# Performance work log

Measured on AMD Instinct MI355X. Metric: run time of the kernel, lower is better.

Reference implementation:

```python
import jax, jax.numpy as jnp
import numpy as np

N_QUBITS = 7
N_LAYERS = 2
DIM = 2 ** N_QUBITS  # 128
NORM_FACTOR = 1.0


def _cnot_gather_idx(n):
    # CNOT chain (0,1),(1,2),...,(n-2,n-1) plus wraparound (n-1,0).
    # new_state[x] = old_state[idx[x]]; apply gates in reverse to arange.
    gates = [(i, i + 1) for i in range(n - 1)] + [(n - 1, 0)]
    idx = np.arange(2 ** n)
    for c, t in reversed(gates):
        cbit = 1 << (n - 1 - c)  # pennylane wire 0 = most significant bit
        tbit = 1 << (n - 1 - t)
        idx = np.where((idx & cbit) > 0, idx ^ tbit, idx)
    return jnp.asarray(idx)

CNOT_IDX = _cnot_gather_idx(N_QUBITS)


def silu(x):
    return x * jax.nn.sigmoid(x)


def cayley(A_real, A_imag):
    # Hermitianize then Cayley transform -> unitary, per layer. [L,D,D]
    A = A_real.astype(jnp.complex64) + 1j * A_imag.astype(jnp.complex64)
    A = A + jnp.conj(jnp.swapaxes(A, -1, -2))
    I = jnp.eye(DIM, dtype=A.dtype)
    return jnp.matmul(A - 1j * I, jnp.linalg.inv(A + 1j * I))


def _single_qubit_gate(theta_x, theta_y):
    # combined G = RY(theta_y) @ RX(theta_x) applied to every qubit
    cx, sx = jnp.cos(theta_x / 2), jnp.sin(theta_x / 2)
    cy, sy = jnp.cos(theta_y / 2), jnp.sin(theta_y / 2)
    RX = jnp.stack([jnp.stack([cx + 0j, -1j * sx]), jnp.stack([-1j * sx, cx + 0j])])
    RY = jnp.stack([jnp.stack([cy + 0j, -sy + 0j]), jnp.stack([sy + 0j, cy + 0j])])
    return RY @ RX


def quantum_evolve(psi, coeffs, q_mats):
    # psi: [N, DIM] complex64 normalized state vectors
    N = psi.shape[0]
    for j in range(N_LAYERS):
        psi = psi @ q_mats[j].T  # QubitUnitary: new = U @ old
        G = _single_qubit_gate(coeffs[j, 0], coeffs[j, 1])
        psi = psi.reshape((N,) + (2,) * N_QUBITS)
        for ax in range(1, N_QUBITS + 1):
            psi = jnp.moveaxis(jnp.tensordot(G, psi, axes=((1,), (ax,))), 0, ax)
        psi = psi.reshape(N, DIM)
        psi = psi[:, CNOT_IDX]  # CNOT chain is a fixed basis permutation
    return psi


def setup_inputs() -> dict:
    key = jax.random.key(0)
    ks = jax.random.split(key, 16)
    N, E = 50000, 800000
    in_nf, hid, out_nf = 128, 128, 128
    h = jax.random.normal(ks[0], (N, in_nf), dtype=jnp.float32)
    edge_index = jax.random.randint(ks[1], (2, E), 0, N)
    s = 0.05
    W_e1 = jax.random.normal(ks[2], (2 * in_nf, hid), dtype=jnp.float32) * s
    b_e1 = jnp.zeros((hid,), dtype=jnp.float32)
    W_e2 = jax.random.normal(ks[3], (hid, hid), dtype=jnp.float32) * s
    b_e2 = jnp.zeros((hid,), dtype=jnp.float32)
    W_enc = jax.random.normal(ks[4], (hid + in_nf, DIM), dtype=jnp.float32) * s
    b_enc = jnp.zeros((DIM,), dtype=jnp.float32)
    coeffs = jax.random.normal(ks[5], (N_LAYERS, 2), dtype=jnp.float32) * 0.1
    A_real = jax.random.normal(ks[6], (N_LAYERS, DIM, DIM), dtype=jnp.float32) * 0.01
    A_imag = jax.random.normal(ks[7], (N_LAYERS, DIM, DIM), dtype=jnp.float32) * 0.01
    W_dec = jax.random.normal(ks[8], (DIM, out_nf), dtype=jnp.float32) * s
    b_dec = jnp.zeros((out_nf,), dtype=jnp.float32)
    return {"h": h, "edge_index": edge_index, "W_e1": W_e1, "b_e1": b_e1,
            "W_e2": W_e2, "b_e2": b_e2, "W_enc": W_enc, "b_enc": b_enc,
            "coeffs": coeffs, "A_real": A_real, "A_imag": A_imag,
            "W_dec": W_dec, "b_dec": b_dec}


def reference(h, edge_index, W_e1, b_e1, W_e2, b_e2, W_enc, b_enc,
              coeffs, A_real, A_imag, W_dec, b_dec):
    row, col = edge_index[0], edge_index[1]
    # edge model: mij = MLP([h_src, h_tgt])
    e = jnp.concatenate([h[row], h[col]], axis=1)  # [E, 2*in_nf]
    e = silu(e @ W_e1 + b_e1)
    edge_feat = silu(e @ W_e2 + b_e2)  # [E, hid]
    # node model: scatter-sum aggregation over destination `row`
    agg = jax.ops.segment_sum(edge_feat, row, num_segments=h.shape[0]) / NORM_FACTOR
    q_input = jnp.concatenate([h, agg], axis=1) @ W_enc + b_enc  # [N, DIM]
    norm = jnp.sqrt(jnp.sum(q_input ** 2, axis=1, keepdims=True) + 1e-12)
    psi = (q_input / norm).astype(jnp.complex64)
    q_mats = cayley(A_real, A_imag)  # [L, DIM, DIM] unitary
    psi = quantum_evolve(psi, coeffs, q_mats)
    out = h + (jnp.real(psi) @ W_dec + b_dec)
    return out, edge_feat
```

## Files before the change

kernel.cpp:

```cpp
#include <hip/hip_runtime.h>
#include <math.h>

#define N_NODES 50000
#define N_EDGES 800000

typedef __attribute__((ext_vector_type(8))) short bf16x8;
typedef __attribute__((ext_vector_type(4))) short bf16x4;
typedef __attribute__((ext_vector_type(2))) short shortx2;
typedef __attribute__((ext_vector_type(4))) float f32x4;

__device__ __forceinline__ float silu_f(float x) {
    float d = 1.0f + __expf(-x);
    return x * __builtin_amdgcn_rcpf(d);
}

__device__ __forceinline__ unsigned short f2bf(float x) {
    union { float f; unsigned u; } v; v.f = x;
    unsigned r = v.u + 0x7FFFu + ((v.u >> 16) & 1u);
    return (unsigned short)(r >> 16);
}

__device__ __forceinline__ void atomic_pk_add_bf16(short* addr, shortx2 v) {
    typedef shortx2 __attribute__((address_space(1)))* gp1;
    __builtin_amdgcn_global_atomic_fadd_v2bf16((gp1)(unsigned long long)addr, v);
}

__global__ __launch_bounds__(256) void prep_kernel(const float* __restrict__ h,
                                                   short* __restrict__ hbf,
                                                   const int* __restrict__ ei,
                                                   int* __restrict__ cnt,
                                                   const float* __restrict__ A_real,
                                                   const float* __restrict__ A_imag,
                                                   float* __restrict__ H,
                                                   float* __restrict__ X) {
    const int bid = blockIdx.x;
    const int t = threadIdx.x;
    if (bid < 3125) {
        int i = bid * 256 + t;
        const float4* h4 = (const float4*)h;
        float4 v0 = h4[i * 2], v1 = h4[i * 2 + 1];
        bf16x8 b;
        b[0] = (short)f2bf(v0.x); b[1] = (short)f2bf(v0.y);
        b[2] = (short)f2bf(v0.z); b[3] = (short)f2bf(v0.w);
        b[4] = (short)f2bf(v1.x); b[5] = (short)f2bf(v1.y);
        b[6] = (short)f2bf(v1.z); b[7] = (short)f2bf(v1.w);
        ((bf16x8*)hbf)[i] = b;
        atomicAdd(&cnt[ei[i]], 1);
    } else {
        int p = bid - 3125;
        int L = p >> 2, q4 = p & 3;
        const float* ar = A_real + L * 16384;
        const float* ai = A_imag + L * 16384;
        float* hre = H + L * 32768;
        float* him = hre + 16384;
        float* xre = X + L * 32768;
        float* xim = xre + 16384;
        for (int m = 0; m < 16; ++m) {
            int idx = q4 * 4096 + t + 256 * m;
            int i = idx >> 7, j = idx & 127;
            float hr = ar[idx] + ar[j * 128 + i];
            float hi = ai[idx] - ai[j * 128 + i];
            hre[idx] = hr;
            him[idx] = hi;
            xre[idx] = hr;
            xim[idx] = hi - (i == j ? 1.0f : 0.0f);
        }
    }
}

__device__ __forceinline__ void ns_t_body(int blk, int t,
                                          const float* __restrict__ H,
                                          const float* __restrict__ X,
                                          float* __restrict__ T) {
    const int L = blk >> 4;
    const int i = (blk & 15) * 8 + (t >> 7);
    const int j = t & 127;
    const float* hre = H + L * 32768;
    const float* him = hre + 16384;
    const float* xre = X + L * 32768;
    const float* xim = xre + 16384;
    float accr = 0.f, acci = 0.f;
    #pragma unroll 4
    for (int k = 0; k < 128; ++k) {
        float hr = hre[i * 128 + k], hi = him[i * 128 + k];
        float xr = xre[k * 128 + j], xi = xim[k * 128 + j];
        accr += hr * xr - hi * xi;
        acci += hr * xi + hi * xr;
    }
    T[L * 32768 + i * 128 + j]          = accr - xim[i * 128 + j];
    T[L * 32768 + 16384 + i * 128 + j]  = acci + xre[i * 128 + j];
}

__device__ __forceinline__ void ns_x_body(int blk, int t,
                                          const float* __restrict__ X,
                                          const float* __restrict__ T,
                                          float* __restrict__ Xout) {
    const int L = blk >> 4;
    const int i = (blk & 15) * 8 + (t >> 7);
    const int j = t & 127;
    const float* xre = X + L * 32768;
    const float* xim = xre + 16384;
    const float* tre = T + L * 32768;
    const float* tim = tre + 16384;
    float accr = 0.f, acci = 0.f;
    #pragma unroll 4
    for (int k = 0; k < 128; ++k) {
        float xr = xre[i * 128 + k], xi = xim[i * 128 + k];
        float tr = tre[k * 128 + j], ti = tim[k * 128 + j];
        accr += xr * tr - xi * ti;
        acci += xr * ti + xi * tr;
    }
    Xout[L * 32768 + i * 128 + j]          = 2.0f * xre[i * 128 + j] - accr;
    Xout[L * 32768 + 16384 + i * 128 + j]  = 2.0f * xim[i * 128 + j] - acci;
}

__global__ __launch_bounds__(1024) void nst_scan_kernel(const float* __restrict__ H,
                                                        const float* __restrict__ X,
                                                        float* __restrict__ T,
                                                        const int* __restrict__ cnt,
                                                        int* __restrict__ cursor) {
    const int bid = blockIdx.x;
    const int t = threadIdx.x;
    if (bid < 32) { ns_t_body(bid, t, H, X, T); return; }
    __shared__ int sA[1024];
    __shared__ int sB[1024];
    const int CH = 49;
    int s = 0;
    #pragma unroll 4
    for (int i = 0; i < CH; ++i) {
        int idx = t * CH + i;
        if (idx < N_NODES) s += cnt[idx];
    }
    sA[t] = s;
    __syncthreads();
    int* src = sA;
    int* dst = sB;
    for (int off = 1; off < 1024; off <<= 1) {
        int v = src[t];
        if (t >= off) v += src[t - off];
        dst[t] = v;
        __syncthreads();
        int* tmp = src; src = dst; dst = tmp;
    }
    int run = (t == 0) ? 0 : src[t - 1];
    for (int i = 0; i < CH; ++i) {
        int idx = t * CH + i;
        if (idx < N_NODES) {
            cursor[idx] = run;
            run += cnt[idx];
        }
    }
}

__global__ __launch_bounds__(1024) void fill_nsx_kernel(const int* __restrict__ ei,
                                                        int* __restrict__ cursor,
                                                        int* __restrict__ elist,
                                                        const float* __restrict__ X,
                                                        const float* __restrict__ T,
                                                        float* __restrict__ Xout) {
    const int bid = blockIdx.x;
    const int t = threadIdx.x;
    if (bid < 782) {
        int e = bid * 1024 + t;
        if (e < N_EDGES) {
            int slot = atomicAdd(&cursor[ei[e]], 1);
            elist[slot] = e;
        }
        return;
    }
    ns_x_body(bid - 782, t, X, T, Xout);
}

__global__ __launch_bounds__(1024) void ns_t_kernel(const float* __restrict__ H,
                                                    const float* __restrict__ X,
                                                    float* __restrict__ T) {
    ns_t_body(blockIdx.x, threadIdx.x, H, X, T);
}

__global__ __launch_bounds__(1024) void ns_x_kernel(const float* __restrict__ X,
                                                    const float* __restrict__ T,
                                                    float* __restrict__ Xout) {
    ns_x_body(blockIdx.x, threadIdx.x, X, T, Xout);
}

__global__ __launch_bounds__(1024) void gateperm_kernel(const float* __restrict__ X,
                                                        const float* __restrict__ coeffs,
                                                        float* __restrict__ Y) {
    __shared__ float Mre[128 * 129];
    __shared__ float Mim[128 * 129];
    const int L = blockIdx.x;
    const int t = threadIdx.x;
    const float* xre = X + L * 32768;
    const float* xim = xre + 16384;

    for (int q = 0; q < 16; ++q) {
        int idx = t + 1024 * q;
        int i = idx >> 7, j = idx & 127;
        Mre[i * 129 + j] = (i == j ? 1.0f : 0.0f) + 2.0f * xim[idx];
        Mim[i * 129 + j] = -2.0f * xre[idx];
    }
    __syncthreads();

    const float tx = coeffs[2 * L + 0] * 0.5f;
    const float ty = coeffs[2 * L + 1] * 0.5f;
    const float cx = cosf(tx), sx = sinf(tx), cy = cosf(ty), sy = sinf(ty);
    const float G00r = cx * cy, G00i = sx * sy;
    const float G01r = -cx * sy, G01i = -sx * cy;
    const float G10r = cx * sy, G10i = -sx * cy;
    const float G11r = cx * cy, G11i = -sx * sy;

    for (int st = 0; st < 7; ++st) {
        int b = 1 << st;
        #pragma unroll
        for (int p = 0; p < 8; ++p) {
            int pid = t + 1024 * p;
            int col = pid & 127, ph = pid >> 7;
            int i0 = ((ph >> st) << (st + 1)) | (ph & (b - 1));
            int i1 = i0 | b;
            float v0r = Mre[i0 * 129 + col], v0i = Mim[i0 * 129 + col];
            float v1r = Mre[i1 * 129 + col], v1i = Mim[i1 * 129 + col];
            Mre[i0 * 129 + col] = G00r * v0r - G00i * v0i + G01r * v1r - G01i * v1i;
            Mim[i0 * 129 + col] = G00r * v0i + G00i * v0r + G01r * v1i + G01i * v1r;
            Mre[i1 * 129 + col] = G10r * v0r - G10i * v0i + G11r * v1r - G11i * v1i;
            Mim[i1 * 129 + col] = G10r * v0i + G10i * v0r + G11r * v1i + G11i * v1r;
        }
        __syncthreads();
    }

    const int cs[7] = {6, 5, 4, 3, 2, 1, 0};
    const int ts[7] = {0, 6, 5, 4, 3, 2, 1};
    float* yre = Y + L * 32768;
    float* yim = yre + 16384;
    for (int q = 0; q < 16; ++q) {
        int idx = t + 1024 * q;
        int ii_ = idx >> 7, col = idx & 127;
        int s = ii_;
        #pragma unroll
        for (int m = 0; m < 7; ++m) {
            int cbit = 1 << (6 - cs[m]);
            int tbit = 1 << (6 - ts[m]);
            if (s & cbit) s ^= tbit;
        }
        yre[idx] = Mre[s * 129 + col];
        yim[idx] = Mim[s * 129 + col];
    }
}

__global__ __launch_bounds__(512) void combine1_kernel(const float* __restrict__ Y,
                                                       float* __restrict__ ReM) {
    __shared__ float q1r[16384];
    __shared__ float q1i[16384];
    const int t = threadIdx.x;
    const float* q1re = Y;
    const float* q1im = Y + 16384;
    const float* q2re = Y + 32768;
    const float* q2im = Y + 49152;
    for (int q = 0; q < 32; ++q) {
        q1r[t + 512 * q] = q1re[t + 512 * q];
        q1i[t + 512 * q] = q1im[t + 512 * q];
    }
    __syncthreads();
    int i = blockIdx.x * 4 + (t >> 7);
    int j = t & 127;
    float acc = 0.f;
    for (int k = 0; k < 128; ++k) {
        acc += q2re[i * 128 + k] * q1r[k * 128 + j] - q2im[i * 128 + k] * q1i[k * 128 + j];
    }
    ReM[i * 128 + j] = acc;
}

__global__ __launch_bounds__(512) void combine2_kernel(const float* __restrict__ ReM,
                                                       const float* __restrict__ W_dec,
                                                       short* __restrict__ Dt) {
    __shared__ float ml[16384];
    __shared__ float wl[16384];
    const int t = threadIdx.x;
    for (int q = 0; q < 32; ++q) {
        ml[t + 512 * q] = ReM[t + 512 * q];
        wl[t + 512 * q] = W_dec[t + 512 * q];
    }
    __syncthreads();
    int k = blockIdx.x * 4 + (t >> 7);
    int j = t & 127;
    float acc = 0.f;
    for (int i = 0; i < 128; ++i) {
        acc += ml[i * 128 + k] * wl[i * 128 + j];
    }
    Dt[j * 128 + k] = (short)f2bf(acc);
}

__global__ __launch_bounds__(768)
__attribute__((amdgpu_waves_per_eu(3, 3)))
void edge_kernel(const short* __restrict__ hbf,
                 const int* __restrict__ ei,
                 const int* __restrict__ elist,
                 const float* __restrict__ W_e1,
                 const float* __restrict__ b_e1,
                 const float* __restrict__ W_e2,
                 const float* __restrict__ b_e2,
                 float* __restrict__ ef_out,
                 short* __restrict__ agg_bf) {
    __shared__ short w1f[64 * 64 * 8];
    __shared__ short w2f[32 * 64 * 8];
    __shared__ short c1s[12][16 * 68];

    const int t = threadIdx.x;
    const int lane = t & 63;
    const int w = t >> 6;
    const int l15 = lane & 15;
    const int kg = lane >> 4;

    {
        const float4* w1_4 = (const float4*)W_e1;
        for (int idx4 = t; idx4 < 8192; idx4 += 768) {
            int k = idx4 >> 5, j4 = idx4 & 31;
            float4 v = w1_4[idx4];
            int s = k >> 5, kgs = (k >> 3) & 3, e = k & 7;
            int fb = s * 8;
            float vz[4] = {v.x, v.y, v.z, v.w};
            #pragma unroll
            for (int z = 0; z < 4; ++z) {
                int j = j4 * 4 + z;
                int nf = j >> 4, jl = j & 15;
                w1f[((fb + nf) * 64 + kgs * 16 + jl) * 8 + e] = (short)f2bf(vz[z]);
            }
        }
        const float4* w2_4 = (const float4*)W_e2;
        for (int idx4 = t; idx4 < 4096; idx4 += 768) {
            int k = idx4 >> 5, j4 = idx4 & 31;
            float4 v = w2_4[idx4];
            int s2 = k >> 5, kgs = (k >> 3) & 3, e = k & 7;
            int fb = s2 * 8;
            float vz[4] = {v.x, v.y, v.z, v.w};
            #pragma unroll
            for (int z = 0; z < 4; ++z) {
                int j = j4 * 4 + z;
                int nf = j >> 4, jl = j & 15;
                w2f[((fb + nf) * 64 + kgs * 16 + jl) * 8 + e] = (short)f2bf(vz[z]);
            }
        }
    }
    float b1v[8], b2v[8];
    #pragma unroll
    for (int nf = 0; nf < 8; ++nf) {
        b1v[nf] = b_e1[nf * 16 + l15];
        b2v[nf] = b_e2[nf * 16 + l15];
    }
    __syncthreads();

    const bf16x8* hb8 = (const bf16x8*)hbf;
    const bf16x8* w1v = (const bf16x8*)w1f;
    const bf16x8* w2v = (const bf16x8*)w2f;
    short* myc1 = &c1s[w][0];
    const int nt = N_EDGES / 16;
    const int TW = gridDim.x * 12;
    const int wvid = blockIdx.x * 12 + w;
    int tile = (int)(((long long)nt * wvid) / TW);
    const int tend = (int)(((long long)nt * (wvid + 1)) / TW);
    if (tile >= tend) return;

    int el = elist[tile * 16 + l15];
    int ri = ei[el];
    int ci = ei[N_EDGES + el];
    bf16x8 a1[8];
    #pragma unroll
    for (int s = 0; s < 4; ++s) a1[s] = hb8[(size_t)ri * 16 + s * 4 + kg];
    #pragma unroll
    for (int s = 0; s < 4; ++s) a1[4 + s] = hb8[(size_t)ci * 16 + s * 4 + kg];

    bool hn = (tile + 1 < tend);
    int eln = 0, rin = 0, cin = 0;
    if (hn) {
        eln = elist[(tile + 1) * 16 + l15];
        rin = ei[eln];
        cin = ei[N_EDGES + eln];
    }

    float runsum[8];
    #pragma unroll
    for (int nf = 0; nf < 8; ++nf) runsum[nf] = 0.f;

    for (;;) {
        bool hn2 = (tile + 2 < tend);
        int eln2 = 0, rin2 = 0, cin2 = 0;
        if (hn2) {
            eln2 = elist[(tile + 2) * 16 + l15];
            rin2 = ei[eln2];
            cin2 = ei[N_EDGES + eln2];
        }

        f32x4 acc[8];
        #pragma unroll
        for (int nf = 0; nf < 8; ++nf) acc[nf] = (f32x4){0.f, 0.f, 0.f, 0.f};
        #pragma unroll
        for (int s = 0; s < 8; ++s) {
            #pragma unroll
            for (int nf = 0; nf < 8; ++nf) {
                bf16x8 b = w1v[(s * 8 + nf) * 64 + lane];
                acc[nf] = __builtin_amdgcn_mfma_f32_16x16x32_bf16(a1[s], b, acc[nf], 0, 0, 0);
            }
        }

        bf16x8 a1n[8];
        if (hn) {
            #pragma unroll
            for (int s = 0; s < 4; ++s) a1n[s] = hb8[(size_t)rin * 16 + s * 4 + kg];
            #pragma unroll
            for (int s = 0; s < 4; ++s) a1n[4 + s] = hb8[(size_t)cin * 16 + s * 4 + kg];
        }

        f32x4 acc2[8];
        #pragma unroll
        for (int nf = 0; nf < 8; ++nf) acc2[nf] = (f32x4){0.f, 0.f, 0.f, 0.f};
        #pragma unroll
        for (int half = 0; half < 2; ++half) {
            #pragma unroll
            for (int nfh = 0; nfh < 4; ++nfh) {
                int nf = half * 4 + nfh;
                #pragma unroll
                for (int r = 0; r < 4; ++r) {
                    int row = kg * 4 + r;
                    int c = nfh * 16 + l15;
                    myc1[row * 68 + c] = (short)f2bf(silu_f(acc[nf][r] + b1v[nf]));
                }
            }
            #pragma unroll
            for (int s2l = 0; s2l < 2; ++s2l) {
                int k0h = s2l * 32 + kg * 8;
                int base = l15 * 68 + k0h;
                bf16x4 lo = *(const bf16x4*)&myc1[base];
                bf16x4 hi = *(const bf16x4*)&myc1[base + 4];
                bf16x8 a2;
                #pragma unroll
                for (int z = 0; z < 4; ++z) { a2[z] = lo[z]; a2[4 + z] = hi[z]; }
                int s2 = half * 2 + s2l;
                #pragma unroll
                for (int nf = 0; nf < 8; ++nf) {
                    bf16x8 b = w2v[(s2 * 8 + nf) * 64 + lane];
                    acc2[nf] = __builtin_amdgcn_mfma_f32_16x16x32_bf16(a2, b, acc2[nf], 0, 0, 0);
                }
            }
        }

        int rw[4], ew[4];
        #pragma unroll
        for (int r = 0; r < 4; ++r) {
            rw[r] = __shfl(ri, kg * 4 + r);
            ew[r] = __shfl(el, kg * 4 + r);
        }
        int rwn0 = hn ? __shfl(rin, kg * 4) : -1;
        #pragma unroll
        for (int r = 0; r < 4; ++r) {
            float* efp = ef_out + (size_t)ew[r] * 128;
            #pragma unroll
            for (int nf = 0; nf < 8; ++nf) {
                int col = nf * 16 + l15;
                float v = silu_f(acc2[nf][r] + b2v[nf]);
                __builtin_nontemporal_store(v, efp + col);
                runsum[nf] += v;
            }
            bool end = (r < 3) ? (rw[r + 1] != rw[r]) : (rw[3] != rwn0);
            if (end) {
                short* agp = agg_bf + (size_t)rw[r] * 128;
                #pragma unroll
                for (int nf = 0; nf < 8; ++nf) {
                    float vn = __shfl_xor(runsum[nf], 1);
                    if ((l15 & 1) == 0) {
                        shortx2 pk;
                        pk.x = (short)f2bf(runsum[nf]);
                        pk.y = (short)f2bf(vn);
                        atomic_pk_add_bf16(agp + nf * 16 + l15, pk);
                    }
                    runsum[nf] = 0.f;
                }
            }
        }

        if (!hn) break;
        tile += 1;
        el = eln; ri = rin; ci = cin;
        #pragma unroll
        for (int s = 0; s < 8; ++s) a1[s] = a1n[s];
        hn = hn2; eln = eln2; rin = rin2; cin = cin2;
    }
}

__global__ __launch_bounds__(1024)
__attribute__((amdgpu_waves_per_eu(4, 4)))
void node_kernel(const short* __restrict__ hbf,
                 const short* __restrict__ agg_bf,
                 const float* __restrict__ W_enc,
                 const float* __restrict__ b_enc,
                 const short* __restrict__ Dt_bf,
                 const float* __restrict__ b_dec,
                 const float* __restrict__ h,
                 float* __restrict__ out) {
    __shared__ short wef[64 * 64 * 8];
    __shared__ short dtf[32 * 64 * 8];
    __shared__ short c1s[16][16 * 68];

    const int t = threadIdx.x;
    const int lane = t & 63;
    const int w = t >> 6;
    const int l15 = lane & 15;
    const int kg = lane >> 4;

    {
        const float4* we4 = (const float4*)W_enc;
        for (int idx4 = t; idx4 < 8192; idx4 += 1024) {
            int k = idx4 >> 5, j4 = idx4 & 31;
            float4 v = we4[idx4];
            int s = k >> 5, kgs = (k >> 3) & 3, e = k & 7;
            int fb = s * 8;
            float vz[4] = {v.x, v.y, v.z, v.w};
            #pragma unroll
            for (int z = 0; z < 4; ++z) {
                int j = j4 * 4 + z;
                int nf = j >> 4, jl = j & 15;
                wef[((fb + nf) * 64 + kgs * 16 + jl) * 8 + e] = (short)f2bf(vz[z]);
            }
        }
        const bf16x8* dt8 = (const bf16x8*)Dt_bf;
        bf16x8* dtv = (bf16x8*)dtf;
        for (int idx8 = t; idx8 < 2048; idx8 += 1024) {
            int brow = idx8 >> 4, kslot = idx8 & 15;
            int s2 = kslot >> 2, kgs = kslot & 3;
            int nf = brow >> 4, jl = brow & 15;
            dtv[(s2 * 8 + nf) * 64 + kgs * 16 + jl] = dt8[idx8];
        }
    }
    float bj1[8], bj2[8];
    #pragma unroll
    for (int nf = 0; nf < 8; ++nf) {
        bj1[nf] = b_enc[nf * 16 + l15];
        bj2[nf] = b_dec[nf * 16 + l15];
    }
    __syncthreads();

    const bf16x8* hb8 = (const bf16x8*)hbf;
    const bf16x8* ab8 = (const bf16x8*)agg_bf;
    const bf16x8* wev = (const bf16x8*)wef;
    const bf16x8* dtv = (const bf16x8*)dtf;
    short* myc1 = &c1s[w][0];
    const int nt = N_NODES / 16;
    const int tile = blockIdx.x * 16 + w;
    if (tile >= nt) return;

    const int node = tile * 16 + l15;
    bf16x8 a[8];
    #pragma unroll
    for (int s = 0; s < 4; ++s) a[s] = hb8[(size_t)node * 16 + s * 4 + kg];
    #pragma unroll
    for (int s = 0; s < 4; ++s) a[4 + s] = ab8[(size_t)node * 16 + s * 4 + kg];

    f32x4 acc[8];
    #pragma unroll
    for (int nf = 0; nf < 8; ++nf) acc[nf] = (f32x4){0.f, 0.f, 0.f, 0.f};
    #pragma unroll
    for (int s = 0; s < 8; ++s) {
        #pragma unroll
        for (int nf = 0; nf < 8; ++nf) {
            bf16x8 b = wev[(s * 8 + nf) * 64 + lane];
            acc[nf] = __builtin_amdgcn_mfma_f32_16x16x32_bf16(a[s], b, acc[nf], 0, 0, 0);
        }
    }

    float nr[4] = {0.f, 0.f, 0.f, 0.f};
    #pragma unroll
    for (int nf = 0; nf < 8; ++nf) {
        #pragma unroll
        for (int r = 0; r < 4; ++r) {
            acc[nf][r] += bj1[nf];
            nr[r] += acc[nf][r] * acc[nf][r];
        }
    }
    #pragma unroll
    for (int r = 0; r < 4; ++r) {
        nr[r] += __shfl_xor(nr[r], 1);
        nr[r] += __shfl_xor(nr[r], 2);
        nr[r] += __shfl_xor(nr[r], 4);
        nr[r] += __shfl_xor(nr[r], 8);
        nr[r] = 1.0f / sqrtf(nr[r] + 1e-12f);
    }

    f32x4 acc2[8];
    #pragma unroll
    for (int nf = 0; nf < 8; ++nf) acc2[nf] = (f32x4){0.f, 0.f, 0.f, 0.f};
    #pragma unroll
    for (int half = 0; half < 2; ++half) {
        #pragma unroll
        for (int nfh = 0; nfh < 4; ++nfh) {
            int nf = half * 4 + nfh;
            #pragma unroll
            for (int r = 0; r < 4; ++r) {
                int row = kg * 4 + r;
                int c = nfh * 16 + l15;
                myc1[row * 68 + c] = (short)f2bf(acc[nf][r] * nr[r]);
            }
        }
        #pragma unroll
        for (int s2l = 0; s2l < 2; ++s2l) {
            int k0h = s2l * 32 + kg * 8;
            int base = l15 * 68 + k0h;
            bf16x4 lo = *(const bf16x4*)&myc1[base];
            bf16x4 hi = *(const bf16x4*)&myc1[base + 4];
            bf16x8 a2;
            #pragma unroll
            for (int z = 0; z < 4; ++z) { a2[z] = lo[z]; a2[4 + z] = hi[z]; }
            int s2 = half * 2 + s2l;
            #pragma unroll
            for (int nf = 0; nf < 8; ++nf) {
                bf16x8 b = dtv[(s2 * 8 + nf) * 64 + lane];
                acc2[nf] = __builtin_amdgcn_mfma_f32_16x16x32_bf16(a2, b, acc2[nf], 0, 0, 0);
            }
        }
    }

    #pragma unroll
    for (int r = 0; r < 4; ++r) {
        size_t rowb = (size_t)(tile * 16 + kg * 4 + r) * 128;
        #pragma unroll
        for (int nf = 0; nf < 8; ++nf) {
            int col = nf * 16 + l15;
            out[rowb + col] = h[rowb + col] + acc2[nf][r] + bj2[nf];
        }
    }
}

extern "C" void kernel_launch(void* const* d_in, const int* in_sizes, int n_in,
                              void* d_out, int out_size, void* d_ws, size_t ws_size,
                              hipStream_t stream) {
    const float* h      = (const float*)d_in[0];
    const int*   ei     = (const int*)d_in[1];
    const float* W_e1   = (const float*)d_in[2];
    const float* b_e1   = (const float*)d_in[3];
    const float* W_e2   = (const float*)d_in[4];
    const float* b_e2   = (const float*)d_in[5];
    const float* W_enc  = (const float*)d_in[6];
    const float* b_enc  = (const float*)d_in[7];
    const float* coeffs = (const float*)d_in[8];
    const float* A_real = (const float*)d_in[9];
    const float* A_imag = (const float*)d_in[10];
    const float* W_dec  = (const float*)d_in[11];
    const float* b_dec  = (const float*)d_in[12];

    float* out    = (float*)d_out;
    float* ef_out = out + (size_t)N_NODES * 128;

    short* agg_bf = (short*)d_ws;
    int*   cnt    = (int*)(agg_bf + (size_t)N_NODES * 128);
    short* h_bf   = (short*)(cnt + 50176);
    int*   cursor = (int*)(h_bf + (size_t)N_NODES * 128);
    int*   elist  = cursor + 50176;
    float* small  = (float*)(elist + N_EDGES);
    float* Ybuf   = small;
    float* ReM    = Ybuf + 65536;
    float* Hbuf   = ReM + 16384;
    float* Xa     = Hbuf + 65536;
    float* Xb     = Xa + 65536;
    float* Tbuf   = Xb + 65536;
    short* Dt_bf  = (short*)(Tbuf + 65536);

    hipMemsetAsync(agg_bf, 0, (size_t)N_NODES * 128 * sizeof(short) + 50176 * sizeof(int),
                   stream);

    prep_kernel<<<3133, 256, 0, stream>>>(h, h_bf, ei, cnt, A_real, A_imag, Hbuf, Xa);
    nst_scan_kernel<<<33, 1024, 0, stream>>>(Hbuf, Xa, Tbuf, cnt, cursor);
    fill_nsx_kernel<<<814, 1024, 0, stream>>>(ei, cursor, elist, Xa, Tbuf, Xb);
    ns_t_kernel<<<32, 1024, 0, stream>>>(Hbuf, Xb, Tbuf);
    ns_x_kernel<<<32, 1024, 0, stream>>>(Xb, Tbuf, Xa);

    gateperm_kernel<<<2, 1024, 0, stream>>>(Xa, coeffs, Ybuf);
    combine1_kernel<<<32, 512, 0, stream>>>(Ybuf, ReM);
    combine2_kernel<<<32, 512, 0, stream>>>(ReM, W_dec, Dt_bf);

    edge_kernel<<<256, 768, 0, stream>>>(h_bf, ei, elist, W_e1, b_e1, W_e2, b_e2,
                                         ef_out, agg_bf);

    node_kernel<<<196, 1024, 0, stream>>>(h_bf, agg_bf, W_enc, b_enc, Dt_bf, b_dec, h, out);
}
```

Baseline: 593.6 us.

## Process two 16-edge tiles per wave in edge kernel to reuse weight fragments

Each wave now handles 32 edges per iteration as two interleaved 16-row MFMA tiles, so every LDS weight fragment load feeds two MFMAs instead of one. The block shrinks from 12 to 8 waves with waves_per_eu lowered to 2, giving more registers per wave. The previous one-tile-ahead prefetch of node feature rows is dropped: gathers now load at the top of each iteration, and only the next tile's edge indices are prefetched. This exposes more gather latency and lowers occupancy in exchange for halving LDS weight traffic per edge.

```diff
diff --git a/kernel.cpp b/kernel.cpp
--- a/kernel.cpp
+++ b/kernel.cpp
@@ -289,8 +289,8 @@
     Dt[j * 128 + k] = (short)f2bf(acc);
 }
 
-__global__ __launch_bounds__(768)
-__attribute__((amdgpu_waves_per_eu(3, 3)))
+__global__ __launch_bounds__(512)
+__attribute__((amdgpu_waves_per_eu(2, 2)))
 void edge_kernel(const short* __restrict__ hbf,
                  const int* __restrict__ ei,
                  const int* __restrict__ elist,
@@ -302,7 +302,7 @@
                  short* __restrict__ agg_bf) {
     __shared__ short w1f[64 * 64 * 8];
     __shared__ short w2f[32 * 64 * 8];
-    __shared__ short c1s[12][16 * 68];
+    __shared__ short c1s[8][32 * 68];
 
     const int t = threadIdx.x;
     const int lane = t & 63;
@@ -312,7 +312,7 @@
 
     {
         const float4* w1_4 = (const float4*)W_e1;
-        for (int idx4 = t; idx4 < 8192; idx4 += 768) {
+        for (int idx4 = t; idx4 < 8192; idx4 += 512) {
             int k = idx4 >> 5, j4 = idx4 & 31;
             float4 v = w1_4[idx4];
             int s = k >> 5, kgs = (k >> 3) & 3, e = k & 7;
@@ -326,7 +326,7 @@
             }
         }
         const float4* w2_4 = (const float4*)W_e2;
-        for (int idx4 = t; idx4 < 4096; idx4 += 768) {
+        for (int idx4 = t; idx4 < 4096; idx4 += 512) {
             int k = idx4 >> 5, j4 = idx4 & 31;
             float4 v = w2_4[idx4];
             int s2 = k >> 5, kgs = (k >> 3) & 3, e = k & 7;
@@ -352,66 +352,63 @@
     const bf16x8* w1v = (const bf16x8*)w1f;
     const bf16x8* w2v = (const bf16x8*)w2f;
     short* myc1 = &c1s[w][0];
-    const int nt = N_EDGES / 16;
-    const int TW = gridDim.x * 12;
-    const int wvid = blockIdx.x * 12 + w;
+    const int nt = N_EDGES / 32;
+    const int TW = gridDim.x * 8;
+    const int wvid = blockIdx.x * 8 + w;
     int tile = (int)(((long long)nt * wvid) / TW);
     const int tend = (int)(((long long)nt * (wvid + 1)) / TW);
     if (tile >= tend) return;
 
-    int el = elist[tile * 16 + l15];
-    int ri = ei[el];
-    int ci = ei[N_EDGES + el];
-    bf16x8 a1[8];
-    #pragma unroll
-    for (int s = 0; s < 4; ++s) a1[s] = hb8[(size_t)ri * 16 + s * 4 + kg];
-    #pragma unroll
-    for (int s = 0; s < 4; ++s) a1[4 + s] = hb8[(size_t)ci * 16 + s * 4 + kg];
-
-    bool hn = (tile + 1 < tend);
-    int eln = 0, rin = 0, cin = 0;
-    if (hn) {
-        eln = elist[(tile + 1) * 16 + l15];
-        rin = ei[eln];
-        cin = ei[N_EDGES + eln];
-    }
-
-    float runsum[8];
-    #pragma unroll
-    for (int nf = 0; nf < 8; ++nf) runsum[nf] = 0.f;
+    int el0 = elist[tile * 32 + l15];
+    int el1 = elist[tile * 32 + 16 + l15];
+    int ri0 = ei[el0], ci0 = ei[N_EDGES + el0];
+    int ri1 = ei[el1], ci1 = ei[N_EDGES + el1];
+
+    float rs0[8], rs1[8];
+    #pragma unroll
+    for (int nf = 0; nf < 8; ++nf) { rs0[nf] = 0.f; rs1[nf] = 0.f; }
 
     for (;;) {
-        bool hn2 = (tile + 2 < tend);
-        int eln2 = 0, rin2 = 0, cin2 = 0;
-        if (hn2) {
-            eln2 = elist[(tile + 2) * 16 + l15];
-            rin2 = ei[eln2];
-            cin2 = ei[N_EDGES + eln2];
-        }
-
-        f32x4 acc[8];
-        #pragma unroll
-        for (int nf = 0; nf < 8; ++nf) acc[nf] = (f32x4){0.f, 0.f, 0.f, 0.f};
+        bf16x8 aA[8], aB[8];
+        #pragma unroll
+        for (int s = 0; s < 4; ++s) {
+            aA[s]     = hb8[(size_t)ri0 * 16 + s * 4 + kg];
+            aA[4 + s] = hb8[(size_t)ci0 * 16 + s * 4 + kg];
+            aB[s]     = hb8[(size_t)ri1 * 16 + s * 4 + kg];
+            aB[4 + s] = hb8[(size_t)ci1 * 16 + s * 4 + kg];
+        }
+
+        const bool hn = (tile + 1 < tend);
+        int el0n = 0, el1n = 0, ri0n = 0, ci0n = 0, ri1n = 0, ci1n = 0;
+        if (hn) {
+            el0n = elist[(tile + 1) * 32 + l15];
+            el1n = elist[(tile + 1) * 32 + 16 + l15];
+            ri0n = ei[el0n]; ci0n = ei[N_EDGES + el0n];
+            ri1n = ei[el1n]; ci1n = ei[N_EDGES + el1n];
+        }
+
+        f32x4 acc0[8], acc1[8];
+        #pragma unroll
+        for (int nf = 0; nf < 8; ++nf) {
+            acc0[nf] = (f32x4){0.f, 0.f, 0.f, 0.f};
+            acc1[nf] = (f32x4){0.f, 0.f, 0.f, 0.f};
+        }
         #pragma unroll
         for (int s = 0; s < 8; ++s) {
             #pragma unroll
             for (int nf = 0; nf < 8; ++nf) {
                 bf16x8 b = w1v[(s * 8 + nf) * 64 + lane];
-                acc[nf] = __builtin_amdgcn_mfma_f32_16x16x32_bf16(a1[s], b, acc[nf], 0, 0, 0);
-            }
-        }
-
-        bf16x8 a1n[8];
-        if (hn) {
-            #pragma unroll
-            for (int s = 0; s < 4; ++s) a1n[s] = hb8[(size_t)rin * 16 + s * 4 + kg];
-            #pragma unroll
-            for (int s = 0; s < 4; ++s) a1n[4 + s] = hb8[(size_t)cin * 16 + s * 4 + kg];
-        }
-
-        f32x4 acc2[8];
-        #pragma unroll
-        for (int nf = 0; nf < 8; ++nf) acc2[nf] = (f32x4){0.f, 0.f, 0.f, 0.f};
+                acc0[nf] = __builtin_amdgcn_mfma_f32_16x16x32_bf16(aA[s], b, acc0[nf], 0, 0, 0);
+                acc1[nf] = __builtin_amdgcn_mfma_f32_16x16x32_bf16(aB[s], b, acc1[nf], 0, 0, 0);
+            }
+        }
+
+        f32x4 acc20[8], acc21[8];
+        #pragma unroll
+        for (int nf = 0; nf < 8; ++nf) {
+            acc20[nf] = (f32x4){0.f, 0.f, 0.f, 0.f};
+            acc21[nf] = (f32x4){0.f, 0.f, 0.f, 0.f};
+        }
         #pragma unroll
         for (int half = 0; half < 2; ++half) {
             #pragma unroll
@@ -421,67 +418,111 @@
                 for (int r = 0; r < 4; ++r) {
                     int row = kg * 4 + r;
                     int c = nfh * 16 + l15;
-                    myc1[row * 68 + c] = (short)f2bf(silu_f(acc[nf][r] + b1v[nf]));
+                    myc1[row * 68 + c] = (short)f2bf(silu_f(acc0[nf][r] + b1v[nf]));
+                    myc1[(16 + row) * 68 + c] = (short)f2bf(silu_f(acc1[nf][r] + b1v[nf]));
                 }
             }
             #pragma unroll
             for (int s2l = 0; s2l < 2; ++s2l) {
                 int k0h = s2l * 32 + kg * 8;
-                int base = l15 * 68 + k0h;
-                bf16x4 lo = *(const bf16x4*)&myc1[base];
-                bf16x4 hi = *(const bf16x4*)&myc1[base + 4];
-                bf16x8 a2;
+                int base0 = l15 * 68 + k0h;
+                int base1 = (16 + l15) * 68 + k0h;
+                bf16x4 lo0 = *(const bf16x4*)&myc1[base0];
+                bf16x4 hi0 = *(const bf16x4*)&myc1[base0 + 4];
+                bf16x4 lo1 = *(const bf16x4*)&myc1[base1];
+                bf16x4 hi1 = *(const bf16x4*)&myc1[base1 + 4];
+                bf16x8 a20, a21;
                 #pragma unroll
-                for (int z = 0; z < 4; ++z) { a2[z] = lo[z]; a2[4 + z] = hi[z]; }
+                for (int z = 0; z < 4; ++z) {
+                    a20[z] = lo0[z]; a20[4 + z] = hi0[z];
+                    a21[z] = lo1[z]; a21[4 + z] = hi1[z];
+                }
                 int s2 = half * 2 + s2l;
                 #pragma unroll
                 for (int nf = 0; nf < 8; ++nf) {
                     bf16x8 b = w2v[(s2 * 8 + nf) * 64 + lane];
-                    acc2[nf] = __builtin_amdgcn_mfma_f32_16x16x32_bf16(a2, b, acc2[nf], 0, 0, 0);
+                    acc20[nf] = __builtin_amdgcn_mfma_f32_16x16x32_bf16(a20, b, acc20[nf], 0, 0, 0);
+                    acc21[nf] = __builtin_amdgcn_mfma_f32_16x16x32_bf16(a21, b, acc21[nf], 0, 0, 0);
                 }
             }
         }
 
-        int rw[4], ew[4];
-        #pragma unroll
-        for (int r = 0; r < 4; ++r) {
-            rw[r] = __shfl(ri, kg * 4 + r);
-            ew[r] = __shfl(el, kg * 4 + r);
-        }
-        int rwn0 = hn ? __shfl(rin, kg * 4) : -1;
-        #pragma unroll
-        for (int r = 0; r < 4; ++r) {
-            float* efp = ef_out + (size_t)ew[r] * 128;
-            #pragma unroll
-            for (int nf = 0; nf < 8; ++nf) {
-                int col = nf * 16 + l15;
-                float v = silu_f(acc2[nf][r] + b2v[nf]);
-                __builtin_nontemporal_store(v, efp + col);
-                runsum[nf] += v;
-            }
-            bool end = (r < 3) ? (rw[r + 1] != rw[r]) : (rw[3] != rwn0);
-            if (end) {
-                short* agp = agg_bf + (size_t)rw[r] * 128;
+        {
+            int rw_[4], ew_[4];
+            #pragma unroll
+            for (int r = 0; r < 4; ++r) {
+                rw_[r] = __shfl(ri0, kg * 4 + r);
+                ew_[r] = __shfl(el0, kg * 4 + r);
+            }
+            int rwn0 = hn ? __shfl(ri0n, kg * 4) : -1;
+            #pragma unroll
+            for (int r = 0; r < 4; ++r) {
+                float* efp = ef_out + (size_t)ew_[r] * 128;
                 #pragma unroll
                 for (int nf = 0; nf < 8; ++nf) {
-                    float vn = __shfl_xor(runsum[nf], 1);
-                    if ((l15 & 1) == 0) {
-                        shortx2 pk;
-                        pk.x = (short)f2bf(runsum[nf]);
-                        pk.y = (short)f2bf(vn);
-                        atomic_pk_add_bf16(agp + nf * 16 + l15, pk);
+                    int col = nf * 16 + l15;
+                    float v = silu_f(acc20[nf][r] + b2v[nf]);
+                    __builtin_nontemporal_store(v, efp + col);
+                    rs0[nf] += v;
+                }
+                bool end = (r < 3) ? (rw_[r + 1] != rw_[r]) : (rw_[3] != rwn0);
+                if (end) {
+                    short* agp = agg_bf + (size_t)rw_[r] * 128;
+                    #pragma unroll
+                    for (int nf = 0; nf < 8; ++nf) {
+                        float vn = __shfl_xor(rs0[nf], 1);
+                        if ((l15 & 1) == 0) {
+                            shortx2 pk;
+                            pk.x = (short)f2bf(rs0[nf]);
+                            pk.y = (short)f2bf(vn);
+                            atomic_pk_add_bf16(agp + nf * 16 + l15, pk);
+                        }
+                        rs0[nf] = 0.f;
                     }
-                    runsum[nf] = 0.f;
+                }
+            }
+        }
+        {
+            int rw_[4], ew_[4];
+            #pragma unroll
+            for (int r = 0; r < 4; ++r) {
+                rw_[r] = __shfl(ri1, kg * 4 + r);
+                ew_[r] = __shfl(el1, kg * 4 + r);
+            }
+            int rwn0 = hn ? __shfl(ri1n, kg * 4) : -1;
+            #pragma unroll
+            for (int r = 0; r < 4; ++r) {
+                float* efp = ef_out + (size_t)ew_[r] * 128;
+                #pragma unroll
+                for (int nf = 0; nf < 8; ++nf) {
+                    int col = nf * 16 + l15;
+                    float v = silu_f(acc21[nf][r] + b2v[nf]);
+                    __builtin_nontemporal_store(v, efp + col);
+                    rs1[nf] += v;
+                }
+                bool end = (r < 3) ? (rw_[r + 1] != rw_[r]) : (rw_[3] != rwn0);
+                if (end) {
+                    short* agp = agg_bf + (size_t)rw_[r] * 128;
+                    #pragma unroll
+                    for (int nf = 0; nf < 8; ++nf) {
+                        float vn = __shfl_xor(rs1[nf], 1);
+                        if ((l15 & 1) == 0) {
+                            shortx2 pk;
+                            pk.x = (short)f2bf(rs1[nf]);
+                            pk.y = (short)f2bf(vn);
+                            atomic_pk_add_bf16(agp + nf * 16 + l15, pk);
+                        }
+                        rs1[nf] = 0.f;
+                    }
                 }
             }
         }
 
         if (!hn) break;
         tile += 1;
-        el = eln; ri = rin; ci = cin;
-        #pragma unroll
-        for (int s = 0; s < 8; ++s) a1[s] = a1n[s];
-        hn = hn2; eln = eln2; rin = rin2; cin = cin2;
+        el0 = el0n; el1 = el1n;
+        ri0 = ri0n; ci0 = ci0n;
+        ri1 = ri1n; ci1 = ci1n;
     }
 }
 
@@ -674,7 +715,7 @@
     combine1_kernel<<<32, 512, 0, stream>>>(Ybuf, ReM);
     combine2_kernel<<<32, 512, 0, stream>>>(ReM, W_dec, Dt_bf);
 
-    edge_kernel<<<256, 768, 0, stream>>>(h_bf, ei, elist, W_e1, b_e1, W_e2, b_e2,
+    edge_kernel<<<256, 512, 0, stream>>>(h_bf, ei, elist, W_e1, b_e1, W_e2, b_e2,
                                          ef_out, agg_bf);
 
     node_kernel<<<196, 1024, 0, stream>>>(h_bf, agg_bf, W_enc, b_enc, Dt_bf, b_dec, h, out);
```

Result: slower. 686.7 us (+15.7%).
